# Optimization experiments

Measured on AMD Instinct MI355X. Metric: run time of the kernel, lower is better.

Reference implementation:

```python
import jax, jax.numpy as jnp
import numpy as np

B, W, H, C = 8, 32, 32, 64   # batch, width, height, hidden_size
NH = 8                        # num_attention_heads
M = 32                        # max_position_embeddings
P = C // 2                    # position_embedding_size (query_positional_score=True)


def setup_inputs() -> dict:
    key = jax.random.key(0)
    ks = jax.random.split(key, 7)
    s = 0.02
    return {
        "hidden_states": jax.random.normal(ks[0], (B, W, H, C), dtype=jnp.float32),
        "row_emb": jax.random.normal(ks[1], (2 * M - 1, P), dtype=jnp.float32) * s,
        "col_emb": jax.random.normal(ks[2], (2 * M - 1, P), dtype=jnp.float32) * s,
        "Wq": jax.random.normal(ks[3], (NH * C, C), dtype=jnp.float32) * s,
        "bq": jnp.zeros((NH * C,), dtype=jnp.float32),
        "Wk": jax.random.normal(ks[4], (NH * C, C), dtype=jnp.float32) * s,
        "bk": jnp.zeros((NH * C,), dtype=jnp.float32),
        "Wv": jax.random.normal(ks[5], (C, NH * C), dtype=jnp.float32) * s,
        "bv": jnp.zeros((C,), dtype=jnp.float32),
    }


def reference(hidden_states, row_emb, col_emb, Wq, bq, Wk, bk, Wv, bv):
    b, w, h, c = hidden_states.shape
    nh = Wq.shape[0] // c
    half = c // 2
    center = row_emb.shape[0] // 2  # = max_position_embeddings - 1

    # projections: all_head_size = nh * c (per source: hidden_size * num_heads)
    q = (hidden_states @ Wq.T + bq).reshape(b, w, h, nh, c)
    k = (hidden_states @ Wk.T + bk).reshape(b, w, h, nh, c)

    # relative index tables: rel[i, j] = (j - i) + (M - 1)
    iw = jnp.arange(w)
    ih = jnp.arange(h)
    rel_w = iw[None, :] - iw[:, None] + center   # (w, w)
    rel_h = ih[None, :] - ih[:, None] + center   # (h, h)
    r_emb = row_emb[rel_w]  # (w, w, P)
    c_emb = col_emb[rel_h]  # (h, h, P)

    # positional scores: q split into row/col halves
    q_row = q[..., :half]
    q_col = q[..., half:]
    row_scores = jnp.einsum('bijhd,ikd->bijhk', q_row, r_emb)  # (b,w,h,nh,w)
    col_scores = jnp.einsum('bijhd,jld->bijhl', q_col, c_emb)  # (b,w,h,nh,h)
    scale = jnp.sqrt(jnp.asarray(c, dtype=hidden_states.dtype))
    scores = (row_scores[..., :, None] + col_scores[..., None, :]) / scale  # (b,w,h,nh,w,h)

    # content scores q^T k
    scores = scores + jnp.einsum('bijhd,bklhd->bijhkl', q, k) / scale

    # softmax over merged spatial key dims (k,l)
    probs = jax.nn.softmax(scores.reshape(b, w, h, nh, w * h), axis=-1).reshape(scores.shape)

    # value mixing directly with hidden_states, then output projection
    mixed = jnp.einsum('bijhkl,bkld->bijhd', probs, hidden_states).reshape(b, w, h, nh * c)
    return mixed @ Wv.T + bv
```

## Files before the change

kernel.cpp:

```cpp
#include <hip/hip_runtime.h>
#include <math.h>

typedef __bf16 bf16;
typedef bf16 bf16x2 __attribute__((ext_vector_type(2)));
typedef bf16 bf16x4 __attribute__((ext_vector_type(4)));
typedef bf16 bf16x8 __attribute__((ext_vector_type(8)));
typedef float f32x4 __attribute__((ext_vector_type(4)));

constexpr int CENTER = 31;
constexpr float QSCALE = 0.125f * 1.4426950408889634f;

static __device__ __forceinline__ unsigned short f2bf_bits(float f) {
    bf16 b = (bf16)f;
    return __builtin_bit_cast(unsigned short, b);
}

static __device__ __forceinline__ float fast_exp2(float x) {
#if __has_builtin(__builtin_amdgcn_exp2f)
    return __builtin_amdgcn_exp2f(x);
#else
    return exp2f(x);
#endif
}

__global__ __launch_bounds__(256)
void prep_kernel(const float* __restrict__ hid,
                 const float* __restrict__ Wq, const float* __restrict__ Wk,
                 const float* __restrict__ Wv,
                 bf16* __restrict__ hb, bf16* __restrict__ htb,
                 bf16* __restrict__ Wqb, bf16* __restrict__ Wkb,
                 bf16* __restrict__ Wvp)
{
    __shared__ __attribute__((aligned(16))) bf16 hs[64][72];

    const int t   = threadIdx.x;
    const int blk = blockIdx.x;
    const int b   = blk >> 4, kc = blk & 15;

    {
        int row = t >> 2, c4 = (t & 3) * 16;
        const float4* src = (const float4*)(hid + ((size_t)b * 1024 + kc * 64 + row) * 64 + c4);
        bf16 tmp[16];
        #pragma unroll
        for (int u = 0; u < 4; ++u) {
            float4 v = src[u];
            tmp[4*u+0] = (bf16)v.x; tmp[4*u+1] = (bf16)v.y;
            tmp[4*u+2] = (bf16)v.z; tmp[4*u+3] = (bf16)v.w;
        }
        *(int4*)&hs[row][c4]     = ((int4*)tmp)[0];
        *(int4*)&hs[row][c4 + 8] = ((int4*)tmp)[1];
        bf16* hdst = hb + ((size_t)b * 1024 + kc * 64 + row) * 64 + c4;
        *(int4*)hdst       = ((int4*)tmp)[0];
        *(int4*)(hdst + 8) = ((int4*)tmp)[1];
    }

    {
        int idx = blk * 256 + t;
        if (idx < 8192) {
            float4 vq = ((const float4*)Wq)[idx];
            float4 vk = ((const float4*)Wk)[idx];
            float4 vv = ((const float4*)Wv)[idx];
            ushort4 pq, pk2, pv;
            pq.x = f2bf_bits(vq.x); pq.y = f2bf_bits(vq.y); pq.z = f2bf_bits(vq.z); pq.w = f2bf_bits(vq.w);
            pk2.x = f2bf_bits(vk.x); pk2.y = f2bf_bits(vk.y); pk2.z = f2bf_bits(vk.z); pk2.w = f2bf_bits(vk.w);
            pv.x = f2bf_bits(vv.x); pv.y = f2bf_bits(vv.y); pv.z = f2bf_bits(vv.z); pv.w = f2bf_bits(vv.w);
            ((ushort4*)Wqb)[idx] = pq;
            ((ushort4*)Wkb)[idx] = pk2;
            int c = idx >> 7, o4 = (idx & 127) * 4;
            size_t dst = (size_t)((c >> 4) * 16 + (o4 >> 5)) * 512 + (c & 15) * 32 + (o4 & 31);
            *(ushort4*)(Wvp + dst) = pv;
        }
    }
    __syncthreads();

    {
        int d = t >> 2, p0 = (t & 3) * 16;
        ushort tmp[16];
        #pragma unroll
        for (int i = 0; i < 16; ++i)
            tmp[i] = __builtin_bit_cast(unsigned short, hs[p0 + i][d]);
        bf16* dst = htb + ((size_t)b * 64 + d) * 1024 + kc * 64 + p0;
        *(int4*)dst       = ((int4*)tmp)[0];
        *(int4*)(dst + 8) = ((int4*)tmp)[1];
    }
}

__global__ __launch_bounds__(256)
void qkproj_kernel(const bf16* __restrict__ hb,
                   const bf16* __restrict__ Wqb, const float* __restrict__ bq,
                   const bf16* __restrict__ Wkb, const float* __restrict__ bk,
                   bf16* __restrict__ qb, bf16* __restrict__ kb)
{
    __shared__ __attribute__((aligned(16))) bf16 As[128][72];
    __shared__ __attribute__((aligned(16))) bf16 Bqs[128][72];
    __shared__ __attribute__((aligned(16))) bf16 Bks[128][72];

    const int t  = threadIdx.x;
    const int pt = blockIdx.x;
    const int ot = blockIdx.y;
    const int p0 = pt * 128;
    const int b  = p0 >> 10;

    {
        int row = t >> 1, ch = (t & 1) * 32;
        const int4* asrc = (const int4*)(hb + (size_t)(p0 + row) * 64 + ch);
        const int4* qsrc = (const int4*)(Wqb + (size_t)(ot * 128 + row) * 64 + ch);
        const int4* ksrc = (const int4*)(Wkb + (size_t)(ot * 128 + row) * 64 + ch);
        #pragma unroll
        for (int u = 0; u < 4; ++u) {
            *(int4*)&As[row][ch + u * 8]  = asrc[u];
            *(int4*)&Bqs[row][ch + u * 8] = qsrc[u];
            *(int4*)&Bks[row][ch + u * 8] = ksrc[u];
        }
    }
    __syncthreads();

    const int w = t >> 6, ln = t & 63, l15 = ln & 15, quad = ln >> 4;

    bf16x8 a[2][2];
    #pragma unroll
    for (int mt = 0; mt < 2; ++mt) {
        a[mt][0] = *(const bf16x8*)&As[w * 32 + mt * 16 + l15][quad * 8];
        a[mt][1] = *(const bf16x8*)&As[w * 32 + mt * 16 + l15][32 + quad * 8];
    }

    const f32x4 z4 = {0.f, 0.f, 0.f, 0.f};

    for (int z = 0; z < 2; ++z) {
        const bf16 (* __restrict__ Bs)[72] = z ? Bks : Bqs;
        const float* bias = z ? bk : bq;
        bf16* outp        = z ? kb : qb;
        const float scale = z ? 1.0f : QSCALE;

        f32x4 acc[2][8];
        #pragma unroll
        for (int mt = 0; mt < 2; ++mt)
            #pragma unroll
            for (int nt = 0; nt < 8; ++nt) acc[mt][nt] = z4;

        #pragma unroll
        for (int nt = 0; nt < 8; ++nt) {
            bf16x8 b0 = *(const bf16x8*)&Bs[nt * 16 + l15][quad * 8];
            bf16x8 b1 = *(const bf16x8*)&Bs[nt * 16 + l15][32 + quad * 8];
            #pragma unroll
            for (int mt = 0; mt < 2; ++mt) {
                acc[mt][nt] = __builtin_amdgcn_mfma_f32_16x16x32_bf16(a[mt][0], b0, acc[mt][nt], 0, 0, 0);
                acc[mt][nt] = __builtin_amdgcn_mfma_f32_16x16x32_bf16(a[mt][1], b1, acc[mt][nt], 0, 0, 0);
            }
        }

        #pragma unroll
        for (int nt = 0; nt < 8; ++nt) {
            int o = ot * 128 + nt * 16 + l15;
            float bv = bias[o];
            int hh = o >> 6, d = o & 63;
            #pragma unroll
            for (int mt = 0; mt < 2; ++mt)
                #pragma unroll
                for (int r = 0; r < 4; ++r) {
                    int pos = (p0 & 1023) + w * 32 + mt * 16 + quad * 4 + r;
                    float val = (acc[mt][nt][r] + bv) * scale;
                    outp[(((size_t)b * 8 + hh) * 1024 + pos) * 64 + d] = (bf16)val;
                }
        }
    }
}

__global__ __launch_bounds__(256)
void bias_kernel(const bf16* __restrict__ qb,
                 const float* __restrict__ row_emb, const float* __restrict__ col_emb,
                 bf16* __restrict__ rowbias, bf16* __restrict__ colbias)
{
    __shared__ __attribute__((aligned(16))) bf16 embRs[63][40];
    __shared__ __attribute__((aligned(16))) bf16 embCs[63][40];

    const int t  = threadIdx.x;
    const int bh = blockIdx.x;
    const int sg = blockIdx.y;

    for (int i = t; i < 2016; i += 256) embRs[i >> 5][i & 31] = (bf16)row_emb[i];
    for (int i = t; i < 2016; i += 256) embCs[i >> 5][i & 31] = (bf16)col_emb[i];
    __syncthreads();

    const int w = t >> 6, ln = t & 63, l15 = ln & 15, quad = ln >> 4;

    #pragma unroll
    for (int u = 0; u < 4; ++u) {
        int s = sg * 16 + u * 4 + w;
        bool cm = s >= 32;
        int ij = cm ? s - 32 : s;

        bf16x8 a[2];
        #pragma unroll
        for (int mt = 0; mt < 2; ++mt) {
            const bf16* ap = cm
                ? qb + ((size_t)bh * 1024 + (mt * 16 + l15) * 32 + ij) * 64 + 32 + quad * 8
                : qb + ((size_t)bh * 1024 + ij * 32 + mt * 16 + l15) * 64 + quad * 8;
            a[mt] = *(const bf16x8*)ap;
        }
        bf16* ob = cm ? colbias : rowbias;

        #pragma unroll
        for (int nt = 0; nt < 2; ++nt) {
            int erow = nt * 16 + l15 + CENTER - ij;
            bf16x8 bfrag = cm ? *(const bf16x8*)&embCs[erow][quad * 8]
                              : *(const bf16x8*)&embRs[erow][quad * 8];
            #pragma unroll
            for (int mt = 0; mt < 2; ++mt) {
                f32x4 c = {0.f, 0.f, 0.f, 0.f};
                c = __builtin_amdgcn_mfma_f32_16x16x32_bf16(a[mt], bfrag, c, 0, 0, 0);
                #pragma unroll
                for (int r = 0; r < 4; ++r) {
                    int ql = mt * 16 + quad * 4 + r;
                    int qrow = cm ? ql * 32 + ij : ij * 32 + ql;
                    ob[((size_t)bh * 1024 + qrow) * 32 + nt * 16 + l15] = (bf16)c[r];
                }
            }
        }
    }
}

__global__ __launch_bounds__(256, 2)
void attn_kernel(const bf16* __restrict__ qb, const bf16* __restrict__ kb,
                 const bf16* __restrict__ htb,
                 const bf16* __restrict__ rowbias, const bf16* __restrict__ colbias,
                 bf16* __restrict__ mixedb)
{
    __shared__ __attribute__((aligned(16))) bf16 Ks[64][72];
    __shared__ __attribute__((aligned(16))) bf16 Hts[64][72];
    __shared__ __attribute__((aligned(16))) bf16 Pp[4][32][72];

    const int t  = threadIdx.x;
    const int qt = blockIdx.x;
    const int bh = blockIdx.y;
    const int b  = bh >> 3, h = bh & 7;
    const int q0 = qt * 128;
    const int w = t >> 6, ln = t & 63, l15 = ln & 15, quad = ln >> 4;

    bf16x8 bq_[2][2];
    float  cbv[2][2][4];
    const bf16* rbp[2];
    #pragma unroll
    for (int mt = 0; mt < 2; ++mt) {
        int qrow = q0 + w * 32 + mt * 16 + l15;
        const bf16* qp = qb + ((size_t)bh * 1024 + qrow) * 64;
        bq_[mt][0] = *(const bf16x8*)(qp + quad * 8);
        bq_[mt][1] = *(const bf16x8*)(qp + 32 + quad * 8);
        #pragma unroll
        for (int par = 0; par < 2; ++par) {
            bf16x4 cv = *(const bf16x4*)(colbias + ((size_t)bh * 1024 + qrow) * 32 + par * 16 + quad * 4);
            #pragma unroll
            for (int r = 0; r < 4; ++r) cbv[mt][par][r] = (float)cv[r];
        }
        rbp[mt] = rowbias + ((size_t)bh * 1024 + qrow) * 32;
    }

    const f32x4 z4 = {0.f, 0.f, 0.f, 0.f};
    f32x4 oacc[2][4];
    float lsum[2] = {0.f, 0.f};
    #pragma unroll
    for (int mt = 0; mt < 2; ++mt)
        #pragma unroll
        for (int dt = 0; dt < 4; ++dt) oacc[mt][dt] = z4;

    bf16* Pw = &Pp[w][0][0];
    const bf16* kcbase = kb + (size_t)bh * 1024 * 64;
    const bf16* hcbase = htb + (size_t)b * 64 * 1024;

    const int srow = t >> 2, sc = (t & 3) << 4;
    const bf16* kptr = kcbase + (size_t)srow * 64 + sc;
    const bf16* hptr = hcbase + (size_t)srow * 1024 + sc;

    int4 kr0 = *(const int4*)(kptr);
    int4 kr1 = *(const int4*)(kptr + 8);
    int4 hr0 = *(const int4*)(hptr);
    int4 hr1 = *(const int4*)(hptr + 8);
    bf16x2 rnext[2];
    #pragma unroll
    for (int mt = 0; mt < 2; ++mt) rnext[mt] = *(const bf16x2*)(rbp[mt]);

    for (int kc = 0; kc < 16; ++kc) {
        __syncthreads();
        *(int4*)&Ks[srow][sc]      = kr0;
        *(int4*)&Ks[srow][sc + 8]  = kr1;
        *(int4*)&Hts[srow][sc]     = hr0;
        *(int4*)&Hts[srow][sc + 8] = hr1;
        float rb[2][2];
        #pragma unroll
        for (int mt = 0; mt < 2; ++mt) {
            rb[mt][0] = (float)rnext[mt][0];
            rb[mt][1] = (float)rnext[mt][1];
        }
        __syncthreads();

        if (kc < 15) {
            const bf16* kn = kptr + (size_t)(kc + 1) * 4096;
            const bf16* hn = hptr + (size_t)(kc + 1) * 64;
            kr0 = *(const int4*)(kn);
            kr1 = *(const int4*)(kn + 8);
            hr0 = *(const int4*)(hn);
            hr1 = *(const int4*)(hn + 8);
            #pragma unroll
            for (int mt = 0; mt < 2; ++mt)
                rnext[mt] = *(const bf16x2*)(rbp[mt] + (kc + 1) * 2);
        }

        f32x4 sf[2][4];
        #pragma unroll
        for (int mt = 0; mt < 2; ++mt)
            #pragma unroll
            for (int kt = 0; kt < 4; ++kt) sf[mt][kt] = z4;
        __builtin_amdgcn_s_setprio(1);
        #pragma unroll
        for (int kt = 0; kt < 4; ++kt) {
            bf16x8 aK0 = *(const bf16x8*)&Ks[kt * 16 + l15][quad * 8];
            bf16x8 aK1 = *(const bf16x8*)&Ks[kt * 16 + l15][32 + quad * 8];
            #pragma unroll
            for (int mt = 0; mt < 2; ++mt) {
                sf[mt][kt] = __builtin_amdgcn_mfma_f32_16x16x32_bf16(aK0, bq_[mt][0], sf[mt][kt], 0, 0, 0);
                sf[mt][kt] = __builtin_amdgcn_mfma_f32_16x16x32_bf16(aK1, bq_[mt][1], sf[mt][kt], 0, 0, 0);
            }
        }
        __builtin_amdgcn_s_setprio(0);

        #pragma unroll
        for (int mt = 0; mt < 2; ++mt)
            #pragma unroll
            for (int kt = 0; kt < 4; ++kt) {
                float rbv = rb[mt][kt >> 1];
                ushort4 pk;
                float p0 = fast_exp2(sf[mt][kt][0] + rbv + cbv[mt][kt & 1][0]);
                float p1 = fast_exp2(sf[mt][kt][1] + rbv + cbv[mt][kt & 1][1]);
                float p2 = fast_exp2(sf[mt][kt][2] + rbv + cbv[mt][kt & 1][2]);
                float p3 = fast_exp2(sf[mt][kt][3] + rbv + cbv[mt][kt & 1][3]);
                lsum[mt] += (p0 + p1) + (p2 + p3);
                pk.x = f2bf_bits(p0); pk.y = f2bf_bits(p1);
                pk.z = f2bf_bits(p2); pk.w = f2bf_bits(p3);
                *(ushort4*)&Pw[(mt * 16 + l15) * 72 + kt * 16 + quad * 4] = pk;
            }

        bf16x8 bp[2][2];
        #pragma unroll
        for (int mt = 0; mt < 2; ++mt) {
            bp[mt][0] = *(const bf16x8*)&Pw[(mt * 16 + l15) * 72 + quad * 8];
            bp[mt][1] = *(const bf16x8*)&Pw[(mt * 16 + l15) * 72 + 32 + quad * 8];
        }
        __builtin_amdgcn_s_setprio(1);
        #pragma unroll
        for (int dt = 0; dt < 4; ++dt) {
            bf16x8 aH0 = *(const bf16x8*)&Hts[dt * 16 + l15][quad * 8];
            bf16x8 aH1 = *(const bf16x8*)&Hts[dt * 16 + l15][32 + quad * 8];
            #pragma unroll
            for (int mt = 0; mt < 2; ++mt) {
                oacc[mt][dt] = __builtin_amdgcn_mfma_f32_16x16x32_bf16(aH0, bp[mt][0], oacc[mt][dt], 0, 0, 0);
                oacc[mt][dt] = __builtin_amdgcn_mfma_f32_16x16x32_bf16(aH1, bp[mt][1], oacc[mt][dt], 0, 0, 0);
            }
        }
        __builtin_amdgcn_s_setprio(0);
    }

    float inv[2];
    #pragma unroll
    for (int mt = 0; mt < 2; ++mt) {
        float v = lsum[mt];
        v += __shfl_xor(v, 16);
        v += __shfl_xor(v, 32);
        inv[mt] = 1.0f / v;
    }
    #pragma unroll
    for (int mt = 0; mt < 2; ++mt) {
        int pos = q0 + w * 32 + mt * 16 + l15;
        bf16* mb = mixedb + ((size_t)b * 1024 + pos) * 512 + h * 64;
        #pragma unroll
        for (int dt = 0; dt < 4; ++dt) {
            ushort4 pk;
            pk.x = f2bf_bits(oacc[mt][dt][0] * inv[mt]);
            pk.y = f2bf_bits(oacc[mt][dt][1] * inv[mt]);
            pk.z = f2bf_bits(oacc[mt][dt][2] * inv[mt]);
            pk.w = f2bf_bits(oacc[mt][dt][3] * inv[mt]);
            *(ushort4*)(mb + dt * 16 + quad * 4) = pk;
        }
    }
}

__global__ __launch_bounds__(256)
void out_proj_kernel(const bf16* __restrict__ mixedb,
                     const bf16* __restrict__ Wvp, const float* __restrict__ bv,
                     float* __restrict__ out)
{
    const int t  = threadIdx.x;
    const int p0 = blockIdx.x * 32;
    const int w = t >> 6, ln = t & 63, l15 = ln & 15, quad = ln >> 4;

    float bvv = bv[w * 16 + l15];
    f32x4 acc[2] = {(f32x4){bvv, bvv, bvv, bvv}, (f32x4){bvv, bvv, bvv, bvv}};

    const bf16* arow0 = mixedb + (size_t)(p0 + l15) * 512 + quad * 8;
    const bf16* arow1 = mixedb + (size_t)(p0 + 16 + l15) * 512 + quad * 8;
    const bf16* bbase = Wvp + (size_t)w * 16 * 512 + l15 * 32 + quad * 8;

    #pragma unroll
    for (int kc = 0; kc < 16; ++kc) {
        bf16x8 a0 = *(const bf16x8*)(arow0 + kc * 32);
        bf16x8 a1 = *(const bf16x8*)(arow1 + kc * 32);
        bf16x8 bfrag = *(const bf16x8*)(bbase + kc * 512);
        acc[0] = __builtin_amdgcn_mfma_f32_16x16x32_bf16(a0, bfrag, acc[0], 0, 0, 0);
        acc[1] = __builtin_amdgcn_mfma_f32_16x16x32_bf16(a1, bfrag, acc[1], 0, 0, 0);
    }

    #pragma unroll
    for (int mt = 0; mt < 2; ++mt)
        #pragma unroll
        for (int r = 0; r < 4; ++r)
            out[(size_t)(p0 + mt * 16 + quad * 4 + r) * 64 + w * 16 + l15] = acc[mt][r];
}

extern "C" void kernel_launch(void* const* d_in, const int* in_sizes, int n_in,
                              void* d_out, int out_size, void* d_ws, size_t ws_size,
                              hipStream_t stream)
{
    const float* hid     = (const float*)d_in[0];
    const float* row_emb = (const float*)d_in[1];
    const float* col_emb = (const float*)d_in[2];
    const float* Wq      = (const float*)d_in[3];
    const float* bq      = (const float*)d_in[4];
    const float* Wk      = (const float*)d_in[5];
    const float* bk      = (const float*)d_in[6];
    const float* Wv      = (const float*)d_in[7];
    const float* bv      = (const float*)d_in[8];
    float* out = (float*)d_out;

    bf16* qb      = (bf16*)d_ws;
    bf16* kb      = qb + (size_t)64 * 1024 * 64;
    bf16* htb     = kb + (size_t)64 * 1024 * 64;
    bf16* rowbias = htb + (size_t)8 * 64 * 1024;
    bf16* colbias = rowbias + (size_t)64 * 1024 * 32;
    bf16* mixedb  = colbias + (size_t)64 * 1024 * 32;
    bf16* hb      = mixedb + (size_t)8 * 1024 * 512;
    bf16* Wqb     = hb + (size_t)8 * 1024 * 64;
    bf16* Wkb     = Wqb + (size_t)512 * 64;
    bf16* Wvp     = Wkb + (size_t)512 * 64;

    prep_kernel<<<128, 256, 0, stream>>>(hid, Wq, Wk, Wv, hb, htb, Wqb, Wkb, Wvp);
    qkproj_kernel<<<dim3(64, 4), 256, 0, stream>>>(hb, Wqb, bq, Wkb, bk, qb, kb);
    bias_kernel<<<dim3(64, 4), 256, 0, stream>>>(qb, row_emb, col_emb, rowbias, colbias);
    attn_kernel<<<dim3(8, 64), 256, 0, stream>>>(qb, kb, htb, rowbias, colbias, mixedb);
    out_proj_kernel<<<256, 256, 0, stream>>>(mixedb, Wvp, bv, out);
}
```

Measured before the change: 125.5 us.

## Halve per-block work across all kernels to double grid sizes and occupancy

Splits Q/K projection across a third grid dimension, halves the rows per block in the bias, attention and output-projection kernels, and doubles each grid to match. The attention kernel now has each wave handle 16 query rows instead of 32, which lowers register and LDS use so launch_bounds can ask for 4 blocks per CU. The goal is more blocks and waves in flight to fill the GPU's CUs on this small problem. The cost is that each staged K/H tile is reused across fewer query rows, so global and LDS traffic per unit of work goes up.

```diff
diff --git a/kernel.cpp b/kernel.cpp
--- a/kernel.cpp
+++ b/kernel.cpp
@@ -92,25 +92,28 @@
                    bf16* __restrict__ qb, bf16* __restrict__ kb)
 {
     __shared__ __attribute__((aligned(16))) bf16 As[128][72];
-    __shared__ __attribute__((aligned(16))) bf16 Bqs[128][72];
-    __shared__ __attribute__((aligned(16))) bf16 Bks[128][72];
+    __shared__ __attribute__((aligned(16))) bf16 Bs[128][72];
 
     const int t  = threadIdx.x;
     const int pt = blockIdx.x;
     const int ot = blockIdx.y;
+    const int z  = blockIdx.z;
     const int p0 = pt * 128;
     const int b  = p0 >> 10;
+
+    const bf16* Wb        = z ? Wkb : Wqb;
+    const float* bias     = z ? bk : bq;
+    bf16* outp            = z ? kb : qb;
+    const float scale     = z ? 1.0f : QSCALE;
 
     {
         int row = t >> 1, ch = (t & 1) * 32;
         const int4* asrc = (const int4*)(hb + (size_t)(p0 + row) * 64 + ch);
-        const int4* qsrc = (const int4*)(Wqb + (size_t)(ot * 128 + row) * 64 + ch);
-        const int4* ksrc = (const int4*)(Wkb + (size_t)(ot * 128 + row) * 64 + ch);
+        const int4* bsrc = (const int4*)(Wb + (size_t)(ot * 128 + row) * 64 + ch);
         #pragma unroll
         for (int u = 0; u < 4; ++u) {
-            *(int4*)&As[row][ch + u * 8]  = asrc[u];
-            *(int4*)&Bqs[row][ch + u * 8] = qsrc[u];
-            *(int4*)&Bks[row][ch + u * 8] = ksrc[u];
+            *(int4*)&As[row][ch + u * 8] = asrc[u];
+            *(int4*)&Bs[row][ch + u * 8] = bsrc[u];
         }
     }
     __syncthreads();
@@ -125,44 +128,36 @@
     }
 
     const f32x4 z4 = {0.f, 0.f, 0.f, 0.f};
-
-    for (int z = 0; z < 2; ++z) {
-        const bf16 (* __restrict__ Bs)[72] = z ? Bks : Bqs;
-        const float* bias = z ? bk : bq;
-        bf16* outp        = z ? kb : qb;
-        const float scale = z ? 1.0f : QSCALE;
-
-        f32x4 acc[2][8];
+    f32x4 acc[2][8];
+    #pragma unroll
+    for (int mt = 0; mt < 2; ++mt)
+        #pragma unroll
+        for (int nt = 0; nt < 8; ++nt) acc[mt][nt] = z4;
+
+    #pragma unroll
+    for (int nt = 0; nt < 8; ++nt) {
+        bf16x8 b0 = *(const bf16x8*)&Bs[nt * 16 + l15][quad * 8];
+        bf16x8 b1 = *(const bf16x8*)&Bs[nt * 16 + l15][32 + quad * 8];
+        #pragma unroll
+        for (int mt = 0; mt < 2; ++mt) {
+            acc[mt][nt] = __builtin_amdgcn_mfma_f32_16x16x32_bf16(a[mt][0], b0, acc[mt][nt], 0, 0, 0);
+            acc[mt][nt] = __builtin_amdgcn_mfma_f32_16x16x32_bf16(a[mt][1], b1, acc[mt][nt], 0, 0, 0);
+        }
+    }
+
+    #pragma unroll
+    for (int nt = 0; nt < 8; ++nt) {
+        int o = ot * 128 + nt * 16 + l15;
+        float bv = bias[o];
+        int hh = o >> 6, d = o & 63;
         #pragma unroll
         for (int mt = 0; mt < 2; ++mt)
             #pragma unroll
-            for (int nt = 0; nt < 8; ++nt) acc[mt][nt] = z4;
-
-        #pragma unroll
-        for (int nt = 0; nt < 8; ++nt) {
-            bf16x8 b0 = *(const bf16x8*)&Bs[nt * 16 + l15][quad * 8];
-            bf16x8 b1 = *(const bf16x8*)&Bs[nt * 16 + l15][32 + quad * 8];
-            #pragma unroll
-            for (int mt = 0; mt < 2; ++mt) {
-                acc[mt][nt] = __builtin_amdgcn_mfma_f32_16x16x32_bf16(a[mt][0], b0, acc[mt][nt], 0, 0, 0);
-                acc[mt][nt] = __builtin_amdgcn_mfma_f32_16x16x32_bf16(a[mt][1], b1, acc[mt][nt], 0, 0, 0);
+            for (int r = 0; r < 4; ++r) {
+                int pos = (p0 & 1023) + w * 32 + mt * 16 + quad * 4 + r;
+                float val = (acc[mt][nt][r] + bv) * scale;
+                outp[(((size_t)b * 8 + hh) * 1024 + pos) * 64 + d] = (bf16)val;
             }
-        }
-
-        #pragma unroll
-        for (int nt = 0; nt < 8; ++nt) {
-            int o = ot * 128 + nt * 16 + l15;
-            float bv = bias[o];
-            int hh = o >> 6, d = o & 63;
-            #pragma unroll
-            for (int mt = 0; mt < 2; ++mt)
-                #pragma unroll
-                for (int r = 0; r < 4; ++r) {
-                    int pos = (p0 & 1023) + w * 32 + mt * 16 + quad * 4 + r;
-                    float val = (acc[mt][nt][r] + bv) * scale;
-                    outp[(((size_t)b * 8 + hh) * 1024 + pos) * 64 + d] = (bf16)val;
-                }
-        }
     }
 }
 
@@ -185,8 +180,8 @@
     const int w = t >> 6, ln = t & 63, l15 = ln & 15, quad = ln >> 4;
 
     #pragma unroll
-    for (int u = 0; u < 4; ++u) {
-        int s = sg * 16 + u * 4 + w;
+    for (int u = 0; u < 2; ++u) {
+        int s = sg * 8 + u * 4 + w;
         bool cm = s >= 32;
         int ij = cm ? s - 32 : s;
 
@@ -220,7 +215,7 @@
     }
 }
 
-__global__ __launch_bounds__(256, 2)
+__global__ __launch_bounds__(256, 4)
 void attn_kernel(const bf16* __restrict__ qb, const bf16* __restrict__ kb,
                  const bf16* __restrict__ htb,
                  const bf16* __restrict__ rowbias, const bf16* __restrict__ colbias,
@@ -228,40 +223,34 @@
 {
     __shared__ __attribute__((aligned(16))) bf16 Ks[64][72];
     __shared__ __attribute__((aligned(16))) bf16 Hts[64][72];
-    __shared__ __attribute__((aligned(16))) bf16 Pp[4][32][72];
+    __shared__ __attribute__((aligned(16))) bf16 Pp[4][16][72];
 
     const int t  = threadIdx.x;
     const int qt = blockIdx.x;
     const int bh = blockIdx.y;
     const int b  = bh >> 3, h = bh & 7;
-    const int q0 = qt * 128;
+    const int q0 = qt * 64;
     const int w = t >> 6, ln = t & 63, l15 = ln & 15, quad = ln >> 4;
 
-    bf16x8 bq_[2][2];
-    float  cbv[2][2][4];
-    const bf16* rbp[2];
-    #pragma unroll
-    for (int mt = 0; mt < 2; ++mt) {
-        int qrow = q0 + w * 32 + mt * 16 + l15;
-        const bf16* qp = qb + ((size_t)bh * 1024 + qrow) * 64;
-        bq_[mt][0] = *(const bf16x8*)(qp + quad * 8);
-        bq_[mt][1] = *(const bf16x8*)(qp + 32 + quad * 8);
-        #pragma unroll
-        for (int par = 0; par < 2; ++par) {
-            bf16x4 cv = *(const bf16x4*)(colbias + ((size_t)bh * 1024 + qrow) * 32 + par * 16 + quad * 4);
-            #pragma unroll
-            for (int r = 0; r < 4; ++r) cbv[mt][par][r] = (float)cv[r];
-        }
-        rbp[mt] = rowbias + ((size_t)bh * 1024 + qrow) * 32;
-    }
+    const int qrow = q0 + w * 16 + l15;
+    const bf16* qp = qb + ((size_t)bh * 1024 + qrow) * 64;
+    bf16x8 bq0 = *(const bf16x8*)(qp + quad * 8);
+    bf16x8 bq1 = *(const bf16x8*)(qp + 32 + quad * 8);
+
+    float cbv[2][4];
+    #pragma unroll
+    for (int par = 0; par < 2; ++par) {
+        bf16x4 cv = *(const bf16x4*)(colbias + ((size_t)bh * 1024 + qrow) * 32 + par * 16 + quad * 4);
+        #pragma unroll
+        for (int r = 0; r < 4; ++r) cbv[par][r] = (float)cv[r];
+    }
+    const bf16* rbp = rowbias + ((size_t)bh * 1024 + qrow) * 32;
 
     const f32x4 z4 = {0.f, 0.f, 0.f, 0.f};
-    f32x4 oacc[2][4];
-    float lsum[2] = {0.f, 0.f};
-    #pragma unroll
-    for (int mt = 0; mt < 2; ++mt)
-        #pragma unroll
-        for (int dt = 0; dt < 4; ++dt) oacc[mt][dt] = z4;
+    f32x4 oacc[4];
+    float lsum = 0.f;
+    #pragma unroll
+    for (int dt = 0; dt < 4; ++dt) oacc[dt] = z4;
 
     bf16* Pw = &Pp[w][0][0];
     const bf16* kcbase = kb + (size_t)bh * 1024 * 64;
@@ -275,9 +264,7 @@
     int4 kr1 = *(const int4*)(kptr + 8);
     int4 hr0 = *(const int4*)(hptr);
     int4 hr1 = *(const int4*)(hptr + 8);
-    bf16x2 rnext[2];
-    #pragma unroll
-    for (int mt = 0; mt < 2; ++mt) rnext[mt] = *(const bf16x2*)(rbp[mt]);
+    bf16x2 rnext = *(const bf16x2*)(rbp);
 
     for (int kc = 0; kc < 16; ++kc) {
         __syncthreads();
@@ -285,12 +272,7 @@
         *(int4*)&Ks[srow][sc + 8]  = kr1;
         *(int4*)&Hts[srow][sc]     = hr0;
         *(int4*)&Hts[srow][sc + 8] = hr1;
-        float rb[2][2];
-        #pragma unroll
-        for (int mt = 0; mt < 2; ++mt) {
-            rb[mt][0] = (float)rnext[mt][0];
-            rb[mt][1] = (float)rnext[mt][1];
-        }
+        float rb0 = (float)rnext[0], rb1 = (float)rnext[1];
         __syncthreads();
 
         if (kc < 15) {
@@ -300,84 +282,63 @@
             kr1 = *(const int4*)(kn + 8);
             hr0 = *(const int4*)(hn);
             hr1 = *(const int4*)(hn + 8);
-            #pragma unroll
-            for (int mt = 0; mt < 2; ++mt)
-                rnext[mt] = *(const bf16x2*)(rbp[mt] + (kc + 1) * 2);
-        }
-
-        f32x4 sf[2][4];
-        #pragma unroll
-        for (int mt = 0; mt < 2; ++mt)
-            #pragma unroll
-            for (int kt = 0; kt < 4; ++kt) sf[mt][kt] = z4;
+            rnext = *(const bf16x2*)(rbp + (kc + 1) * 2);
+        }
+
+        f32x4 sf[4];
+        #pragma unroll
+        for (int kt = 0; kt < 4; ++kt) sf[kt] = z4;
         __builtin_amdgcn_s_setprio(1);
         #pragma unroll
         for (int kt = 0; kt < 4; ++kt) {
             bf16x8 aK0 = *(const bf16x8*)&Ks[kt * 16 + l15][quad * 8];
             bf16x8 aK1 = *(const bf16x8*)&Ks[kt * 16 + l15][32 + quad * 8];
-            #pragma unroll
-            for (int mt = 0; mt < 2; ++mt) {
-                sf[mt][kt] = __builtin_amdgcn_mfma_f32_16x16x32_bf16(aK0, bq_[mt][0], sf[mt][kt], 0, 0, 0);
-                sf[mt][kt] = __builtin_amdgcn_mfma_f32_16x16x32_bf16(aK1, bq_[mt][1], sf[mt][kt], 0, 0, 0);
-            }
+            sf[kt] = __builtin_amdgcn_mfma_f32_16x16x32_bf16(aK0, bq0, sf[kt], 0, 0, 0);
+            sf[kt] = __builtin_amdgcn_mfma_f32_16x16x32_bf16(aK1, bq1, sf[kt], 0, 0, 0);
         }
         __builtin_amdgcn_s_setprio(0);
 
         #pragma unroll
-        for (int mt = 0; mt < 2; ++mt)
-            #pragma unroll
-            for (int kt = 0; kt < 4; ++kt) {
-                float rbv = rb[mt][kt >> 1];
-                ushort4 pk;
-                float p0 = fast_exp2(sf[mt][kt][0] + rbv + cbv[mt][kt & 1][0]);
-                float p1 = fast_exp2(sf[mt][kt][1] + rbv + cbv[mt][kt & 1][1]);
-                float p2 = fast_exp2(sf[mt][kt][2] + rbv + cbv[mt][kt & 1][2]);
-                float p3 = fast_exp2(sf[mt][kt][3] + rbv + cbv[mt][kt & 1][3]);
-                lsum[mt] += (p0 + p1) + (p2 + p3);
-                pk.x = f2bf_bits(p0); pk.y = f2bf_bits(p1);
-                pk.z = f2bf_bits(p2); pk.w = f2bf_bits(p3);
-                *(ushort4*)&Pw[(mt * 16 + l15) * 72 + kt * 16 + quad * 4] = pk;
-            }
-
-        bf16x8 bp[2][2];
-        #pragma unroll
-        for (int mt = 0; mt < 2; ++mt) {
-            bp[mt][0] = *(const bf16x8*)&Pw[(mt * 16 + l15) * 72 + quad * 8];
-            bp[mt][1] = *(const bf16x8*)&Pw[(mt * 16 + l15) * 72 + 32 + quad * 8];
-        }
+        for (int kt = 0; kt < 4; ++kt) {
+            float rbv = (kt >> 1) ? rb1 : rb0;
+            ushort4 pk;
+            float p0 = fast_exp2(sf[kt][0] + rbv + cbv[kt & 1][0]);
+            float p1 = fast_exp2(sf[kt][1] + rbv + cbv[kt & 1][1]);
+            float p2 = fast_exp2(sf[kt][2] + rbv + cbv[kt & 1][2]);
+            float p3 = fast_exp2(sf[kt][3] + rbv + cbv[kt & 1][3]);
+            lsum += (p0 + p1) + (p2 + p3);
+            pk.x = f2bf_bits(p0); pk.y = f2bf_bits(p1);
+            pk.z = f2bf_bits(p2); pk.w = f2bf_bits(p3);
+            *(ushort4*)&Pw[l15 * 72 + kt * 16 + quad * 4] = pk;
+        }
+
+        bf16x8 bp0 = *(const bf16x8*)&Pw[l15 * 72 + quad * 8];
+        bf16x8 bp1 = *(const bf16x8*)&Pw[l15 * 72 + 32 + quad * 8];
         __builtin_amdgcn_s_setprio(1);
         #pragma unroll
         for (int dt = 0; dt < 4; ++dt) {
             bf16x8 aH0 = *(const bf16x8*)&Hts[dt * 16 + l15][quad * 8];
             bf16x8 aH1 = *(const bf16x8*)&Hts[dt * 16 + l15][32 + quad * 8];
-            #pragma unroll
-            for (int mt = 0; mt < 2; ++mt) {
-                oacc[mt][dt] = __builtin_amdgcn_mfma_f32_16x16x32_bf16(aH0, bp[mt][0], oacc[mt][dt], 0, 0, 0);
-                oacc[mt][dt] = __builtin_amdgcn_mfma_f32_16x16x32_bf16(aH1, bp[mt][1], oacc[mt][dt], 0, 0, 0);
-            }
+            oacc[dt] = __builtin_amdgcn_mfma_f32_16x16x32_bf16(aH0, bp0, oacc[dt], 0, 0, 0);
+            oacc[dt] = __builtin_amdgcn_mfma_f32_16x16x32_bf16(aH1, bp1, oacc[dt], 0, 0, 0);
         }
         __builtin_amdgcn_s_setprio(0);
     }
 
-    float inv[2];
-    #pragma unroll
-    for (int mt = 0; mt < 2; ++mt) {
-        float v = lsum[mt];
-        v += __shfl_xor(v, 16);
-        v += __shfl_xor(v, 32);
-        inv[mt] = 1.0f / v;
-    }
-    #pragma unroll
-    for (int mt = 0; mt < 2; ++mt) {
-        int pos = q0 + w * 32 + mt * 16 + l15;
-        bf16* mb = mixedb + ((size_t)b * 1024 + pos) * 512 + h * 64;
+    float v = lsum;
+    v += __shfl_xor(v, 16);
+    v += __shfl_xor(v, 32);
+    float inv = 1.0f / v;
+
+    {
+        bf16* mb = mixedb + ((size_t)b * 1024 + qrow) * 512 + h * 64;
         #pragma unroll
         for (int dt = 0; dt < 4; ++dt) {
             ushort4 pk;
-            pk.x = f2bf_bits(oacc[mt][dt][0] * inv[mt]);
-            pk.y = f2bf_bits(oacc[mt][dt][1] * inv[mt]);
-            pk.z = f2bf_bits(oacc[mt][dt][2] * inv[mt]);
-            pk.w = f2bf_bits(oacc[mt][dt][3] * inv[mt]);
+            pk.x = f2bf_bits(oacc[dt][0] * inv);
+            pk.y = f2bf_bits(oacc[dt][1] * inv);
+            pk.z = f2bf_bits(oacc[dt][2] * inv);
+            pk.w = f2bf_bits(oacc[dt][3] * inv);
             *(ushort4*)(mb + dt * 16 + quad * 4) = pk;
         }
     }
@@ -389,30 +350,25 @@
                      float* __restrict__ out)
 {
     const int t  = threadIdx.x;
-    const int p0 = blockIdx.x * 32;
+    const int p0 = blockIdx.x * 16;
     const int w = t >> 6, ln = t & 63, l15 = ln & 15, quad = ln >> 4;
 
     float bvv = bv[w * 16 + l15];
-    f32x4 acc[2] = {(f32x4){bvv, bvv, bvv, bvv}, (f32x4){bvv, bvv, bvv, bvv}};
-
-    const bf16* arow0 = mixedb + (size_t)(p0 + l15) * 512 + quad * 8;
-    const bf16* arow1 = mixedb + (size_t)(p0 + 16 + l15) * 512 + quad * 8;
+    f32x4 acc = {bvv, bvv, bvv, bvv};
+
+    const bf16* arow  = mixedb + (size_t)(p0 + l15) * 512 + quad * 8;
     const bf16* bbase = Wvp + (size_t)w * 16 * 512 + l15 * 32 + quad * 8;
 
     #pragma unroll
     for (int kc = 0; kc < 16; ++kc) {
-        bf16x8 a0 = *(const bf16x8*)(arow0 + kc * 32);
-        bf16x8 a1 = *(const bf16x8*)(arow1 + kc * 32);
+        bf16x8 a0 = *(const bf16x8*)(arow + kc * 32);
         bf16x8 bfrag = *(const bf16x8*)(bbase + kc * 512);
-        acc[0] = __builtin_amdgcn_mfma_f32_16x16x32_bf16(a0, bfrag, acc[0], 0, 0, 0);
-        acc[1] = __builtin_amdgcn_mfma_f32_16x16x32_bf16(a1, bfrag, acc[1], 0, 0, 0);
-    }
-
-    #pragma unroll
-    for (int mt = 0; mt < 2; ++mt)
-        #pragma unroll
-        for (int r = 0; r < 4; ++r)
-            out[(size_t)(p0 + mt * 16 + quad * 4 + r) * 64 + w * 16 + l15] = acc[mt][r];
+        acc = __builtin_amdgcn_mfma_f32_16x16x32_bf16(a0, bfrag, acc, 0, 0, 0);
+    }
+
+    #pragma unroll
+    for (int r = 0; r < 4; ++r)
+        out[(size_t)(p0 + quad * 4 + r) * 64 + w * 16 + l15] = acc[r];
 }
 
 extern "C" void kernel_launch(void* const* d_in, const int* in_sizes, int n_in,
@@ -442,8 +398,8 @@
     bf16* Wvp     = Wkb + (size_t)512 * 64;
 
     prep_kernel<<<128, 256, 0, stream>>>(hid, Wq, Wk, Wv, hb, htb, Wqb, Wkb, Wvp);
-    qkproj_kernel<<<dim3(64, 4), 256, 0, stream>>>(hb, Wqb, bq, Wkb, bk, qb, kb);
-    bias_kernel<<<dim3(64, 4), 256, 0, stream>>>(qb, row_emb, col_emb, rowbias, colbias);
-    attn_kernel<<<dim3(8, 64), 256, 0, stream>>>(qb, kb, htb, rowbias, colbias, mixedb);
-    out_proj_kernel<<<256, 256, 0, stream>>>(mixedb, Wvp, bv, out);
-}
+    qkproj_kernel<<<dim3(64, 4, 2), 256, 0, stream>>>(hb, Wqb, bq, Wkb, bk, qb, kb);
+    bias_kernel<<<dim3(64, 8), 256, 0, stream>>>(qb, row_emb, col_emb, rowbias, colbias);
+    attn_kernel<<<dim3(16, 64), 256, 0, stream>>>(qb, kb, htb, rowbias, colbias, mixedb);
+    out_proj_kernel<<<512, 256, 0, stream>>>(mixedb, Wvp, bv, out);
+}
```

Measured after the change: 195.6 us. 1.56x slower.
